# Kernel tuning notes

Measured on AMD Instinct MI355X. Metric: run time of the kernel, lower is better.

The kernel has to match this reference:

```python
import jax, jax.numpy as jnp
import numpy as np

B, N, M = 64, 1024, 80
C1, D = 288, 256  # object_dim, lang_dim
EPS = 1e-12  # F.normalize eps


def setup_inputs() -> dict:
    key = jax.random.key(0)
    ks = jax.random.split(key, 16)
    w = lambda k, s: jax.random.normal(k, s, jnp.float32) * 0.05
    object_feat = jax.random.normal(ks[0], (B, N, C1), jnp.float32)
    lang_feat = jax.random.normal(ks[1], (B, M, D), jnp.float32)
    lang_mask = jax.random.randint(ks[2], (B, M), 0, 2).astype(jnp.int32)
    lang_mask = lang_mask.at[:, 0].set(1)  # ensure >=1 valid token per row
    return {
        "object_feat": object_feat,
        "lang_feat": lang_feat,
        "lang_mask": lang_mask,
        # object_att_fc: Linear(C1,D) -> ReLU -> Linear(D,D)
        "W1": w(ks[3], (C1, D)), "b1": w(ks[4], (D,)),
        "W2": w(ks[5], (D, D)), "b2": w(ks[6], (D,)),
        # atten_fc: Dropout(eval=identity) -> Linear(2D,1)
        "Wa": w(ks[7], (2 * D, 1)), "ba": w(ks[8], (1,)),
        # object_score_fc: Linear(C1,D) -> ReLU -> Linear(D,D)
        "W3": w(ks[9], (C1, D)), "b3": w(ks[10], (D,)),
        "W4": w(ks[11], (D, D)), "b4": w(ks[12], (D,)),
        # score_fc: Dropout(eval=identity) -> Linear(D,1)
        "Ws": w(ks[13], (D, 1)), "bs": w(ks[14], (1,)),
    }


def reference(object_feat, lang_feat, lang_mask, W1, b1, W2, b2, Wa, ba, W3, b3, W4, b4, Ws, bs):
    # object attention features: (B,N,D)
    oa = jnp.maximum(object_feat @ W1 + b1, 0.0) @ W2 + b2
    # additive attention: cat([oa, lang]) @ Wa == oa @ Wa[:D] + lang @ Wa[D:]
    w_o, w_l = Wa[:D, 0], Wa[D:, 0]
    score = (oa @ w_o)[:, :, None] + (lang_feat @ w_l)[:, None, :] + ba[0]  # (B,N,M)
    score = jnp.where(lang_mask[:, None, :] == 0, -jnp.inf, score)
    att = jax.nn.softmax(score, axis=2)  # (B,N,M)
    att_feat = jnp.einsum("bnm,bmd->bnd", att, lang_feat)  # sum(att * lang_att)
    # object score branch
    osc = jnp.maximum(object_feat @ W3 + b3, 0.0) @ W4 + b4  # (B,N,D)
    x = jnp.maximum(att_feat * osc, 0.0)
    # F.normalize over channel dim (dim=2)
    nrm = jnp.sqrt(jnp.sum(x * x, axis=2, keepdims=True))
    x = x / jnp.maximum(nrm, EPS)
    out = x @ Ws + bs  # (B,N,1)
    return jnp.transpose(out, (0, 2, 1))  # (B,1,N)
```

## Files before the change

### kernel.cpp

```cpp
#include <hip/hip_runtime.h>
#include <math.h>
#include <stdint.h>

#define B_  64
#define N_  1024
#define M_  80
#define C1_ 288
#define D_  256
#define EPS_ 1e-12f

typedef _Float16 f16;
typedef _Float16 f16x8 __attribute__((ext_vector_type(8)));
typedef float    f32x4 __attribute__((ext_vector_type(4)));

#define ATT_OFF 0
#define W3F_OFF 65536
#define W4F_OFF (65536 + 147456)

__device__ __forceinline__ void g2l16(const void* g, void* l) {
    __builtin_amdgcn_global_load_lds(
        (const __attribute__((address_space(1))) uint32_t*)g,
        (__attribute__((address_space(3))) uint32_t*)l, 16, 0, 0);
}

__device__ __forceinline__ uint32_t pk2(float a, float b) {
    union { f16 h[2]; uint32_t u; } c;
    c.h[0] = (f16)a; c.h[1] = (f16)b;
    return c.u;
}

__device__ __forceinline__ f16x8 w4_to_f16x8(uint32_t w0, uint32_t w1,
                                             uint32_t w2, uint32_t w3) {
    union { uint32_t u[4]; f16x8 h; } c;
    c.u[0] = w0; c.u[1] = w1; c.u[2] = w2; c.u[3] = w3;
    return c.h;
}

__global__ __launch_bounds__(256) void prep_kernel(
    const float* __restrict__ lang_feat,
    const int*   __restrict__ lang_mask,
    const float* __restrict__ Wa,
    const float* __restrict__ W3,
    const float* __restrict__ W4,
    float* __restrict__ att_ws,
    f16* __restrict__ w3f, f16* __restrict__ w4f)
{
    const int bi = blockIdx.x;
    if (bi >= B_) {
        const int kb = bi - B_;
        const float* src; f16* dst; int K0;
        if (kb < 9) { src = W3; dst = w3f + kb * 8192;       K0 = kb * 32; }
        else        { src = W4; dst = w4f + (kb - 9) * 8192; K0 = (kb - 9) * 32; }
        for (int idx = threadIdx.x; idx < 8192; idx += 256) {
            int nt  = idx >> 9;
            int rem = idx & 511;
            int ln  = rem >> 3;
            int i   = rem & 7;
            int k   = K0 + ((ln >> 4) << 3) + i;
            int col = (nt << 4) + (ln & 15);
            dst[idx] = (f16)src[k * D_ + col];
        }
        return;
    }

    __shared__ float wl_s[D_];
    __shared__ float ls[M_];
    const int b   = bi;
    const int tid = threadIdx.x;

    wl_s[tid] = Wa[D_ + tid];
    __syncthreads();

    const int wave = tid >> 6, lane = tid & 63;
    for (int m = wave; m < M_; m += 4) {
        const float* lf = lang_feat + (size_t)(b * M_ + m) * D_;
        float p = 0.f;
        #pragma unroll
        for (int j = 0; j < 4; ++j) { int d = lane + 64 * j; p = fmaf(lf[d], wl_s[d], p); }
        #pragma unroll
        for (int off = 32; off; off >>= 1) p += __shfl_xor(p, off);
        if (lane == 0) ls[m] = (lang_mask[b * M_ + m] == 0) ? -INFINITY : p;
    }
    __syncthreads();

    float mx = -INFINITY;
    #pragma unroll
    for (int m0 = 0; m0 < M_; m0 += 8) {
        float v0 = ls[m0], v1 = ls[m0+1], v2 = ls[m0+2], v3 = ls[m0+3];
        float v4 = ls[m0+4], v5 = ls[m0+5], v6 = ls[m0+6], v7 = ls[m0+7];
        mx = fmaxf(mx, fmaxf(fmaxf(fmaxf(v0,v1), fmaxf(v2,v3)),
                             fmaxf(fmaxf(v4,v5), fmaxf(v6,v7))));
    }
    __syncthreads();
    if (tid < M_) ls[tid] = expf(ls[tid] - mx);
    __syncthreads();

    float s0 = 0.f, s1 = 0.f, s2 = 0.f, s3 = 0.f;
    #pragma unroll
    for (int m0 = 0; m0 < M_; m0 += 8) {
        s0 += ls[m0] + ls[m0+4];
        s1 += ls[m0+1] + ls[m0+5];
        s2 += ls[m0+2] + ls[m0+6];
        s3 += ls[m0+3] + ls[m0+7];
    }
    const float inv = 1.f / ((s0 + s1) + (s2 + s3));

    const int d = tid;
    float a0 = 0.f, a1 = 0.f, a2 = 0.f, a3 = 0.f;
    const float* lfb = lang_feat + (size_t)b * M_ * D_ + d;
    #pragma unroll 5
    for (int m = 0; m < M_; m += 4) {
        a0 = fmaf(ls[m],   lfb[(size_t)m * D_],       a0);
        a1 = fmaf(ls[m+1], lfb[(size_t)(m+1) * D_],   a1);
        a2 = fmaf(ls[m+2], lfb[(size_t)(m+2) * D_],   a2);
        a3 = fmaf(ls[m+3], lfb[(size_t)(m+3) * D_],   a3);
    }
    att_ws[b * D_ + d] = ((a0 + a1) + (a2 + a3)) * inv;
}

__global__ __launch_bounds__(512, 2) void main_kernel(
    const float* __restrict__ obj,
    const f16*  __restrict__ w3f,
    const f16*  __restrict__ w4f,
    const float* __restrict__ b3,
    const float* __restrict__ b4,
    const float* __restrict__ Ws,
    const float* __restrict__ bs,
    const float* __restrict__ att,
    float* __restrict__ out)
{
    extern __shared__ char smem[];
    const int tid  = threadIdx.x;
    const int lane = tid & 63;
    const int w    = tid >> 6;
    const int g    = lane & 15;
    const int q    = lane >> 4;

    #pragma unroll
    for (int i = 0; i < 16; ++i) {
        int off = (i * 512 + tid) * 16;
        g2l16((const char*)w4f + off, smem + off);
    }

    const int r0w = (blockIdx.x * 8 + w) * 32;
    const int b   = blockIdx.x >> 2;

    f32x4 acc[2][16];
    #pragma unroll
    for (int nt = 0; nt < 16; ++nt) {
        f32x4 bv = *(const f32x4*)&b3[nt * 16 + q * 4];
        acc[0][nt] = bv; acc[1][nt] = bv;
    }

    const float* ap0 = obj + (size_t)(r0w + g) * C1_ + q * 8;
    const float* ap1 = ap0 + 16 * C1_;

    #pragma unroll 3
    for (int ks = 0; ks < 9; ++ks) {
        float4 p00 = *(const float4*)(ap0 + ks * 32);
        float4 p01 = *(const float4*)(ap0 + ks * 32 + 4);
        float4 p10 = *(const float4*)(ap1 + ks * 32);
        float4 p11 = *(const float4*)(ap1 + ks * 32 + 4);
        f16x8 o0 = {(f16)p00.x,(f16)p00.y,(f16)p00.z,(f16)p00.w,
                    (f16)p01.x,(f16)p01.y,(f16)p01.z,(f16)p01.w};
        f16x8 o1 = {(f16)p10.x,(f16)p10.y,(f16)p10.z,(f16)p10.w,
                    (f16)p11.x,(f16)p11.y,(f16)p11.z,(f16)p11.w};
        const f16* wp = w3f + ks * 8192;
        #pragma unroll
        for (int nt = 0; nt < 16; ++nt) {
            f16x8 wf = *(const f16x8*)(wp + nt * 512 + lane * 8);
            acc[0][nt] = __builtin_amdgcn_mfma_f32_16x16x32_f16(wf, o0, acc[0][nt], 0, 0, 0);
            acc[1][nt] = __builtin_amdgcn_mfma_f32_16x16x32_f16(wf, o1, acc[1][nt], 0, 0, 0);
        }
    }

    uint32_t S[2][16][2];
    #pragma unroll
    for (int h = 0; h < 2; ++h)
        #pragma unroll
        for (int nt = 0; nt < 16; ++nt) {
            S[h][nt][0] = pk2(fmaxf(acc[h][nt][0], 0.f), fmaxf(acc[h][nt][1], 0.f));
            S[h][nt][1] = pk2(fmaxf(acc[h][nt][2], 0.f), fmaxf(acc[h][nt][3], 0.f));
        }

    const int a0 = (g + 32 * (q & 1)) * 4;
    const int a1 = a0 + 64;
    const bool hi = (lane >= 32);
    f16x8 hf[2][8];
    #pragma unroll
    for (int h = 0; h < 2; ++h)
        #pragma unroll
        for (int ks = 0; ks < 8; ++ks) {
            uint32_t wd[4];
            #pragma unroll
            for (int p = 0; p < 4; ++p) {
                int ad = (p >> 1) ? a1 : a0;
                int vA = __builtin_amdgcn_ds_bpermute(ad, (int)S[h][2*ks][p & 1]);
                int vB = __builtin_amdgcn_ds_bpermute(ad, (int)S[h][2*ks+1][p & 1]);
                wd[p] = hi ? (uint32_t)vB : (uint32_t)vA;
            }
            hf[h][ks] = w4_to_f16x8(wd[0], wd[1], wd[2], wd[3]);
        }

    f32x4 acc2[2][16];
    #pragma unroll
    for (int nt = 0; nt < 16; ++nt) {
        f32x4 bv = *(const f32x4*)&b4[nt * 16 + q * 4];
        acc2[0][nt] = bv; acc2[1][nt] = bv;
    }

    __syncthreads();

    #pragma unroll
    for (int ks = 0; ks < 8; ++ks) {
        const char* bp = smem + ks * 16384;
        #pragma unroll
        for (int nt = 0; nt < 16; ++nt) {
            f16x8 wf = *(const f16x8*)&bp[nt * 1024 + lane * 16];
            acc2[0][nt] = __builtin_amdgcn_mfma_f32_16x16x32_f16(wf, hf[0][ks], acc2[0][nt], 0, 0, 0);
            acc2[1][nt] = __builtin_amdgcn_mfma_f32_16x16x32_f16(wf, hf[1][ks], acc2[1][nt], 0, 0, 0);
        }
    }

    const float bsv = bs[0];
    float s2[2] = {0.f, 0.f}, sw[2] = {0.f, 0.f};
    #pragma unroll
    for (int nt = 0; nt < 16; ++nt) {
        f32x4 av = *(const f32x4*)&att[(b << 8) + nt * 16 + q * 4];
        f32x4 wv = *(const f32x4*)&Ws[nt * 16 + q * 4];
        #pragma unroll
        for (int h = 0; h < 2; ++h)
            #pragma unroll
            for (int r = 0; r < 4; ++r) {
                float x = fmaxf(av[r] * acc2[h][nt][r], 0.f);
                s2[h] = fmaf(x, x, s2[h]);
                sw[h] = fmaf(x, wv[r], sw[h]);
            }
    }
    #pragma unroll
    for (int h = 0; h < 2; ++h) {
        s2[h] += __shfl_xor(s2[h], 16);  sw[h] += __shfl_xor(sw[h], 16);
        s2[h] += __shfl_xor(s2[h], 32);  sw[h] += __shfl_xor(sw[h], 32);
    }
    if (lane < 16) {
        out[r0w + g]      = sw[0] / fmaxf(sqrtf(s2[0]), EPS_) + bsv;
        out[r0w + 16 + g] = sw[1] / fmaxf(sqrtf(s2[1]), EPS_) + bsv;
    }
}

extern "C" void kernel_launch(void* const* d_in, const int* in_sizes, int n_in,
                              void* d_out, int out_size, void* d_ws, size_t ws_size,
                              hipStream_t stream) {
    const float* object_feat = (const float*)d_in[0];
    const float* lang_feat   = (const float*)d_in[1];
    const int*   lang_mask   = (const int*)d_in[2];
    const float* Wa = (const float*)d_in[7];
    const float* W3 = (const float*)d_in[9];
    const float* b3 = (const float*)d_in[10];
    const float* W4 = (const float*)d_in[11];
    const float* b4 = (const float*)d_in[12];
    const float* Ws = (const float*)d_in[13];
    const float* bs = (const float*)d_in[14];
    float* out = (float*)d_out;

    char* ws   = (char*)d_ws;
    float* att = (float*)(ws + ATT_OFF);
    f16*  w3f  = (f16*)(ws + W3F_OFF);
    f16*  w4f  = (f16*)(ws + W4F_OFF);

    hipFuncSetAttribute(reinterpret_cast<const void*>(main_kernel),
                        hipFuncAttributeMaxDynamicSharedMemorySize, 131072);

    prep_kernel<<<B_ + 17, 256, 0, stream>>>(lang_feat, lang_mask, Wa, W3, W4,
                                             att, w3f, w4f);
    main_kernel<<<256, 512, 131072, stream>>>(object_feat, w3f, w4f,
                                              b3, b4, Ws, bs, att, out);
}
```

Measured before the change: 174.5 us.

## Stream W3/W4 tiles through a 4-slot LDS ring buffer with halved rows per wave

```diff
diff --git a/kernel.cpp b/kernel.cpp
--- a/kernel.cpp
+++ b/kernel.cpp
@@ -14,8 +14,7 @@
 typedef float    f32x4 __attribute__((ext_vector_type(4)));
 
 #define ATT_OFF 0
-#define W3F_OFF 65536
-#define W4F_OFF (65536 + 147456)
+#define WALL_OFF 65536
 
 __device__ __forceinline__ void g2l16(const void* g, void* l) {
     __builtin_amdgcn_global_load_lds(
@@ -29,12 +28,14 @@
     return c.u;
 }
 
-__device__ __forceinline__ f16x8 w4_to_f16x8(uint32_t w0, uint32_t w1,
-                                             uint32_t w2, uint32_t w3) {
+__device__ __forceinline__ f16x8 mk8(uint32_t w0, uint32_t w1,
+                                     uint32_t w2, uint32_t w3) {
     union { uint32_t u[4]; f16x8 h; } c;
     c.u[0] = w0; c.u[1] = w1; c.u[2] = w2; c.u[3] = w3;
     return c.h;
 }
+
+#define SB() __builtin_amdgcn_sched_barrier(0)
 
 __global__ __launch_bounds__(256) void prep_kernel(
     const float* __restrict__ lang_feat,
@@ -43,14 +44,15 @@
     const float* __restrict__ W3,
     const float* __restrict__ W4,
     float* __restrict__ att_ws,
-    f16* __restrict__ w3f, f16* __restrict__ w4f)
+    f16* __restrict__ wall)
 {
     const int bi = blockIdx.x;
     if (bi >= B_) {
         const int kb = bi - B_;
-        const float* src; f16* dst; int K0;
-        if (kb < 9) { src = W3; dst = w3f + kb * 8192;       K0 = kb * 32; }
-        else        { src = W4; dst = w4f + (kb - 9) * 8192; K0 = (kb - 9) * 32; }
+        const float* src; int K0;
+        if (kb < 9) { src = W3; K0 = kb * 32; }
+        else        { src = W4; K0 = (kb - 9) * 32; }
+        f16* dst = wall + kb * 8192;
         for (int idx = threadIdx.x; idx < 8192; idx += 256) {
             int nt  = idx >> 9;
             int rem = idx & 511;
@@ -118,10 +120,11 @@
     att_ws[b * D_ + d] = ((a0 + a1) + (a2 + a3)) * inv;
 }
 
-__global__ __launch_bounds__(512, 2) void main_kernel(
+#define SLOT 16384
+
+__global__ __launch_bounds__(512, 4) void main_kernel(
     const float* __restrict__ obj,
-    const f16*  __restrict__ w3f,
-    const f16*  __restrict__ w4f,
+    const f16*  __restrict__ wall,
     const float* __restrict__ b3,
     const float* __restrict__ b4,
     const float* __restrict__ Ws,
@@ -129,123 +132,132 @@
     const float* __restrict__ att,
     float* __restrict__ out)
 {
-    extern __shared__ char smem[];
+    __shared__ char smem[4 * SLOT];
     const int tid  = threadIdx.x;
     const int lane = tid & 63;
     const int w    = tid >> 6;
     const int g    = lane & 15;
     const int q    = lane >> 4;
 
-    #pragma unroll
-    for (int i = 0; i < 16; ++i) {
-        int off = (i * 512 + tid) * 16;
-        g2l16((const char*)w4f + off, smem + off);
-    }
-
-    const int r0w = (blockIdx.x * 8 + w) * 32;
-    const int b   = blockIdx.x >> 2;
-
-    f32x4 acc[2][16];
+    const int r0w = (blockIdx.x * 8 + w) * 16;
+    const int b   = r0w >> 10;
+
+#define STAGE(p) do {                                                   \
+        const char* _g = (const char*)wall + (p) * SLOT + tid * 16;     \
+        char* _l = smem + ((p) & 3) * SLOT + tid * 16;                  \
+        g2l16(_g, _l); g2l16(_g + 8192, _l + 8192);                     \
+    } while (0)
+
+    f32x4 acc[16];
+    #pragma unroll
+    for (int nt = 0; nt < 16; ++nt)
+        acc[nt] = *(const f32x4*)&b3[nt * 16 + q * 4];
+
+    STAGE(0); SB();
+    STAGE(1); SB();
+    STAGE(2); SB();
+    const float* ap = obj + (size_t)(r0w + g) * C1_ + q * 8;
+    float4 oc0 = *(const float4*)(ap);
+    float4 oc1 = *(const float4*)(ap + 4);
+    SB();
+
+    #pragma unroll
+    for (int k = 0; k < 9; ++k) {
+        if (k == 0) asm volatile("s_waitcnt vmcnt(4)" ::: "memory");
+        else        asm volatile("s_waitcnt vmcnt(6)" ::: "memory");
+        __builtin_amdgcn_s_barrier();
+        SB();
+        if (k < 8) {
+            float4 on0 = *(const float4*)(ap + (k + 1) * 32);
+            float4 on1 = *(const float4*)(ap + (k + 1) * 32 + 4);
+            SB();
+            STAGE(k + 3);
+            SB();
+            f16x8 o = {(f16)oc0.x,(f16)oc0.y,(f16)oc0.z,(f16)oc0.w,
+                       (f16)oc1.x,(f16)oc1.y,(f16)oc1.z,(f16)oc1.w};
+            const char* bb = smem + (k & 3) * SLOT;
+            #pragma unroll
+            for (int nt = 0; nt < 16; ++nt) {
+                f16x8 wf = *(const f16x8*)&bb[nt * 1024 + lane * 16];
+                acc[nt] = __builtin_amdgcn_mfma_f32_16x16x32_f16(wf, o, acc[nt], 0, 0, 0);
+            }
+            oc0 = on0; oc1 = on1;
+        } else {
+            STAGE(11);
+            SB();
+            f16x8 o = {(f16)oc0.x,(f16)oc0.y,(f16)oc0.z,(f16)oc0.w,
+                       (f16)oc1.x,(f16)oc1.y,(f16)oc1.z,(f16)oc1.w};
+            const char* bb = smem + (k & 3) * SLOT;
+            #pragma unroll
+            for (int nt = 0; nt < 16; ++nt) {
+                f16x8 wf = *(const f16x8*)&bb[nt * 1024 + lane * 16];
+                acc[nt] = __builtin_amdgcn_mfma_f32_16x16x32_f16(wf, o, acc[nt], 0, 0, 0);
+            }
+        }
+    }
+
+    uint32_t S[16][2];
     #pragma unroll
     for (int nt = 0; nt < 16; ++nt) {
-        f32x4 bv = *(const f32x4*)&b3[nt * 16 + q * 4];
-        acc[0][nt] = bv; acc[1][nt] = bv;
-    }
-
-    const float* ap0 = obj + (size_t)(r0w + g) * C1_ + q * 8;
-    const float* ap1 = ap0 + 16 * C1_;
-
-    #pragma unroll 3
-    for (int ks = 0; ks < 9; ++ks) {
-        float4 p00 = *(const float4*)(ap0 + ks * 32);
-        float4 p01 = *(const float4*)(ap0 + ks * 32 + 4);
-        float4 p10 = *(const float4*)(ap1 + ks * 32);
-        float4 p11 = *(const float4*)(ap1 + ks * 32 + 4);
-        f16x8 o0 = {(f16)p00.x,(f16)p00.y,(f16)p00.z,(f16)p00.w,
-                    (f16)p01.x,(f16)p01.y,(f16)p01.z,(f16)p01.w};
-        f16x8 o1 = {(f16)p10.x,(f16)p10.y,(f16)p10.z,(f16)p10.w,
-                    (f16)p11.x,(f16)p11.y,(f16)p11.z,(f16)p11.w};
-        const f16* wp = w3f + ks * 8192;
-        #pragma unroll
-        for (int nt = 0; nt < 16; ++nt) {
-            f16x8 wf = *(const f16x8*)(wp + nt * 512 + lane * 8);
-            acc[0][nt] = __builtin_amdgcn_mfma_f32_16x16x32_f16(wf, o0, acc[0][nt], 0, 0, 0);
-            acc[1][nt] = __builtin_amdgcn_mfma_f32_16x16x32_f16(wf, o1, acc[1][nt], 0, 0, 0);
-        }
-    }
-
-    uint32_t S[2][16][2];
-    #pragma unroll
-    for (int h = 0; h < 2; ++h)
-        #pragma unroll
-        for (int nt = 0; nt < 16; ++nt) {
-            S[h][nt][0] = pk2(fmaxf(acc[h][nt][0], 0.f), fmaxf(acc[h][nt][1], 0.f));
-            S[h][nt][1] = pk2(fmaxf(acc[h][nt][2], 0.f), fmaxf(acc[h][nt][3], 0.f));
-        }
-
+        S[nt][0] = pk2(fmaxf(acc[nt][0], 0.f), fmaxf(acc[nt][1], 0.f));
+        S[nt][1] = pk2(fmaxf(acc[nt][2], 0.f), fmaxf(acc[nt][3], 0.f));
+    }
     const int a0 = (g + 32 * (q & 1)) * 4;
     const int a1 = a0 + 64;
     const bool hi = (lane >= 32);
-    f16x8 hf[2][8];
-    #pragma unroll
-    for (int h = 0; h < 2; ++h)
-        #pragma unroll
-        for (int ks = 0; ks < 8; ++ks) {
-            uint32_t wd[4];
-            #pragma unroll
-            for (int p = 0; p < 4; ++p) {
-                int ad = (p >> 1) ? a1 : a0;
-                int vA = __builtin_amdgcn_ds_bpermute(ad, (int)S[h][2*ks][p & 1]);
-                int vB = __builtin_amdgcn_ds_bpermute(ad, (int)S[h][2*ks+1][p & 1]);
-                wd[p] = hi ? (uint32_t)vB : (uint32_t)vA;
-            }
-            hf[h][ks] = w4_to_f16x8(wd[0], wd[1], wd[2], wd[3]);
-        }
-
-    f32x4 acc2[2][16];
-    #pragma unroll
-    for (int nt = 0; nt < 16; ++nt) {
-        f32x4 bv = *(const f32x4*)&b4[nt * 16 + q * 4];
-        acc2[0][nt] = bv; acc2[1][nt] = bv;
-    }
-
-    __syncthreads();
-
+    f16x8 hf[8];
     #pragma unroll
     for (int ks = 0; ks < 8; ++ks) {
-        const char* bp = smem + ks * 16384;
+        uint32_t wd[4];
+        #pragma unroll
+        for (int p = 0; p < 4; ++p) {
+            int ad = (p >> 1) ? a1 : a0;
+            int vA = __builtin_amdgcn_ds_bpermute(ad, (int)S[2*ks][p & 1]);
+            int vB = __builtin_amdgcn_ds_bpermute(ad, (int)S[2*ks+1][p & 1]);
+            wd[p] = hi ? (uint32_t)vB : (uint32_t)vA;
+        }
+        hf[ks] = mk8(wd[0], wd[1], wd[2], wd[3]);
+    }
+
+    f32x4 acc2[16];
+    #pragma unroll
+    for (int nt = 0; nt < 16; ++nt)
+        acc2[nt] = *(const f32x4*)&b4[nt * 16 + q * 4];
+
+    #pragma unroll
+    for (int j = 0; j < 8; ++j) {
+        if (j < 6)       asm volatile("s_waitcnt vmcnt(4)" ::: "memory");
+        else if (j == 6) asm volatile("s_waitcnt vmcnt(2)" ::: "memory");
+        else             asm volatile("s_waitcnt vmcnt(0)" ::: "memory");
+        __builtin_amdgcn_s_barrier();
+        SB();
+        if (j < 5) { STAGE(12 + j); SB(); }
+        const char* bb = smem + ((9 + j) & 3) * SLOT;
         #pragma unroll
         for (int nt = 0; nt < 16; ++nt) {
-            f16x8 wf = *(const f16x8*)&bp[nt * 1024 + lane * 16];
-            acc2[0][nt] = __builtin_amdgcn_mfma_f32_16x16x32_f16(wf, hf[0][ks], acc2[0][nt], 0, 0, 0);
-            acc2[1][nt] = __builtin_amdgcn_mfma_f32_16x16x32_f16(wf, hf[1][ks], acc2[1][nt], 0, 0, 0);
-        }
-    }
+            f16x8 wf = *(const f16x8*)&bb[nt * 1024 + lane * 16];
+            acc2[nt] = __builtin_amdgcn_mfma_f32_16x16x32_f16(wf, hf[j], acc2[nt], 0, 0, 0);
+        }
+    }
+#undef STAGE
 
     const float bsv = bs[0];
-    float s2[2] = {0.f, 0.f}, sw[2] = {0.f, 0.f};
+    float s2 = 0.f, sw = 0.f;
     #pragma unroll
     for (int nt = 0; nt < 16; ++nt) {
         f32x4 av = *(const f32x4*)&att[(b << 8) + nt * 16 + q * 4];
         f32x4 wv = *(const f32x4*)&Ws[nt * 16 + q * 4];
         #pragma unroll
-        for (int h = 0; h < 2; ++h)
-            #pragma unroll
-            for (int r = 0; r < 4; ++r) {
-                float x = fmaxf(av[r] * acc2[h][nt][r], 0.f);
-                s2[h] = fmaf(x, x, s2[h]);
-                sw[h] = fmaf(x, wv[r], sw[h]);
-            }
-    }
-    #pragma unroll
-    for (int h = 0; h < 2; ++h) {
-        s2[h] += __shfl_xor(s2[h], 16);  sw[h] += __shfl_xor(sw[h], 16);
-        s2[h] += __shfl_xor(s2[h], 32);  sw[h] += __shfl_xor(sw[h], 32);
-    }
-    if (lane < 16) {
-        out[r0w + g]      = sw[0] / fmaxf(sqrtf(s2[0]), EPS_) + bsv;
-        out[r0w + 16 + g] = sw[1] / fmaxf(sqrtf(s2[1]), EPS_) + bsv;
-    }
+        for (int r = 0; r < 4; ++r) {
+            float x = fmaxf(av[r] * acc2[nt][r], 0.f);
+            s2 = fmaf(x, x, s2);
+            sw = fmaf(x, wv[r], sw);
+        }
+    }
+    s2 += __shfl_xor(s2, 16);  sw += __shfl_xor(sw, 16);
+    s2 += __shfl_xor(s2, 32);  sw += __shfl_xor(sw, 32);
+    if (lane < 16)
+        out[r0w + g] = sw / fmaxf(sqrtf(s2), EPS_) + bsv;
 }
 
 extern "C" void kernel_launch(void* const* d_in, const int* in_sizes, int n_in,
@@ -263,16 +275,12 @@
     const float* bs = (const float*)d_in[14];
     float* out = (float*)d_out;
 
-    char* ws   = (char*)d_ws;
-    float* att = (float*)(ws + ATT_OFF);
-    f16*  w3f  = (f16*)(ws + W3F_OFF);
-    f16*  w4f  = (f16*)(ws + W4F_OFF);
-
-    hipFuncSetAttribute(reinterpret_cast<const void*>(main_kernel),
-                        hipFuncAttributeMaxDynamicSharedMemorySize, 131072);
+    char* ws    = (char*)d_ws;
+    float* att  = (float*)(ws + ATT_OFF);
+    f16*  wall  = (f16*)(ws + WALL_OFF);
 
     prep_kernel<<<B_ + 17, 256, 0, stream>>>(lang_feat, lang_mask, Wa, W3, W4,
-                                             att, w3f, w4f);
-    main_kernel<<<256, 512, 131072, stream>>>(object_feat, w3f, w4f,
-                                              b3, b4, Ws, bs, att, out);
-}
+                                             att, wall);
+    main_kernel<<<512, 512, 0, stream>>>(object_feat, wall,
+                                         b3, b4, Ws, bs, att, out);
+}
```

New measurement: 167.7 us. 3.9% less time.
